# Kernel tuning notes

Hardware: AMD Instinct MI355X
Metric: run time of the kernel (lower is better)

Reference implementation:

```python
import jax, jax.numpy as jnp
import numpy as np

B, S, H, NH = 4, 1024, 1024, 16
DH = H // NH
EPS = 1e-12  # BERT layer_norm_eps


def layer_norm(x, scale, bias, eps=EPS):
    mu = jnp.mean(x, axis=-1, keepdims=True)
    var = jnp.var(x, axis=-1, keepdims=True)
    return (x - mu) / jnp.sqrt(var + eps) * scale + bias


def setup_inputs() -> dict:
    key = jax.random.key(0)
    ks = jax.random.split(key, 8)
    lin = lambda k: jax.random.normal(k, (H, H), jnp.float32) * 0.02
    zeros_h = jnp.zeros((H,), jnp.float32)
    return {
        "hidden_states": jax.random.normal(ks[0], (B, S, H), jnp.float32),
        "group_prob": jnp.zeros((B, S, S), jnp.float32),
        "attention_mask": jnp.ones((B, 1, S, S), jnp.int32),
        "Wq": lin(ks[1]), "bq": zeros_h,
        "Wk": lin(ks[2]), "bk": zeros_h,
        "Wv": lin(ks[3]), "bv": zeros_h,
        "gWq": lin(ks[4]), "gbq": zeros_h,
        "gWk": lin(ks[5]), "gbk": zeros_h,
        "g_ln_scale": jnp.ones((H,), jnp.float32), "g_ln_bias": zeros_h,
        "Wo": lin(ks[6]), "bo": zeros_h,
        "out_ln_scale": jnp.ones((H,), jnp.float32), "out_ln_bias": zeros_h,
    }


def _forward(hidden_states, group_prob, attention_mask, Wq, bq, Wk, bk, Wv, bv,
             gWq, gbq, gWk, gbk, g_ln_scale, g_ln_bias, Wo, bo,
             out_ln_scale, out_ln_bias):
    am = attention_mask.astype(jnp.int32)              # [B,1,S,S]
    a = jnp.eye(S, k=1, dtype=jnp.int32)               # superdiagonal
    b = jnp.eye(S, dtype=jnp.int32)                    # identity
    c = jnp.eye(S, k=-1, dtype=jnp.int32)              # subdiagonal
    tri = jnp.triu(jnp.ones((S, S), jnp.float32))      # upper tri incl diag

    # ---- GroupAttention (tree-transformer constituent priors) ----
    hs = layer_norm(hidden_states, g_ln_scale, g_ln_bias)
    gq = hs @ gWq.T + gbq
    gk = hs @ gWk.T + gbk
    g_scores = jnp.einsum('bqd,bkd->bqk', gq, gk) / jnp.float32(H)
    g_mask = (am & (a + c))[:, 0]                      # [B,S,S] tridiag band, no diag
    g_scores = jnp.where(g_mask == 0, -jnp.inf, g_scores)
    n_attn = jnp.nan_to_num(jax.nn.softmax(g_scores, axis=-1))
    n_attn = jnp.sqrt(n_attn * jnp.swapaxes(n_attn, -1, -2) + 1e-9)
    n_attn = group_prob + (1.0 - group_prob) * n_attn  # prior mixing
    t = jnp.where(a == 0, 0.0, jnp.log(n_attn + 1e-9)) @ tri
    g_attn = jnp.exp(tri @ t)
    strict_upper = tri.astype(jnp.int32) - b           # nonzero on strict upper tri
    g_attn = jnp.where(strict_upper == 0, 0.0, g_attn)
    g_attn = g_attn + jnp.swapaxes(g_attn, -1, -2) + jnp.where(b == 0, 1e-9, n_attn)
    break_prob = n_attn

    # ---- BertSelfAttention, mode 'L' ----
    def split_heads(x):
        return x.reshape(B, S, NH, DH).transpose(0, 2, 1, 3)  # [B,NH,S,DH]
    q = split_heads(hidden_states @ Wq.T + bq)
    k = split_heads(hidden_states @ Wk.T + bk)
    v = split_heads(hidden_states @ Wv.T + bv)
    scores = jnp.einsum('bhqd,bhkd->bhqk', q, k) / jnp.sqrt(jnp.float32(DH))
    keep = (am | b) != 0                               # diag always attended
    scores = jnp.where(keep, scores, -jnp.inf)
    probs = jax.nn.softmax(scores, axis=-1)
    probs = probs * g_attn[:, None]                    # group-prob reweighting
    ctx = jnp.einsum('bhqk,bhkd->bhqd', probs, v)
    ctx = ctx.transpose(0, 2, 1, 3).reshape(B, S, H)

    # ---- BertSelfOutput: dense + residual + LayerNorm ----
    out = layer_norm(ctx @ Wo.T + bo + hidden_states, out_ln_scale, out_ln_bias)
    return out, scores, g_attn, break_prob


def reference(hidden_states, group_prob, attention_mask, Wq, bq, Wk, bk, Wv, bv,
              gWq, gbq, gWk, gbk, g_ln_scale, g_ln_bias, Wo, bo,
              out_ln_scale, out_ln_bias):
    return _forward(hidden_states, group_prob, attention_mask, Wq, bq, Wk, bk,
                    Wv, bv, gWq, gbq, gWk, gbk, g_ln_scale, g_ln_bias, Wo, bo,
                    out_ln_scale, out_ln_bias)
```

## Files before the change

kernel.cpp:

```cpp
#include <hip/hip_runtime.h>
#include <math.h>

#define BB 4
#define S 1024
#define H 1024
#define NHD 16
#define DH 64
#define LN_EPS 1e-12f
#define SQ9 3.1622776601683795e-5f
#define NEG_INF (-__builtin_inff())

typedef unsigned short u16;
typedef unsigned int u32;
using bfrag = __attribute__((ext_vector_type(8))) short;
using f32x4 = __attribute__((ext_vector_type(4))) float;

typedef __attribute__((address_space(1))) void void_g;
typedef __attribute__((address_space(3))) void void_l;

__device__ __forceinline__ void gload16(const void* g, void* l) {
  __builtin_amdgcn_global_load_lds((void_g*)g, (void_l*)l, 16, 0, 0);
}

__device__ __forceinline__ u16 f2bf(float f) {
  u32 u = __builtin_bit_cast(u32, f);
  u32 r = (u + 0x7fffu + ((u >> 16) & 1u)) >> 16;
  return (u16)r;
}
__device__ __forceinline__ float bf2f(u32 b) {
  u32 u = b << 16;
  return __builtin_bit_cast(float, u);
}

__device__ __forceinline__ float block_sum256(float v, float* buf) {
#pragma unroll
  for (int o = 32; o > 0; o >>= 1) v += __shfl_down(v, o);
  if ((threadIdx.x & 63) == 0) buf[threadIdx.x >> 6] = v;
  __syncthreads();
  float r = buf[0] + buf[1] + buf[2] + buf[3];
  __syncthreads();
  return r;
}

__global__ __launch_bounds__(256) void cast_all_kernel(
    const float* __restrict__ Wq, const float* __restrict__ Wk, const float* __restrict__ Wv,
    const float* __restrict__ gWq, const float* __restrict__ gWk, const float* __restrict__ Wo,
    const float* __restrict__ hidden, u16* __restrict__ dst) {
  const int WQ = (H * H) / 4;
  int i = blockIdx.x * 256 + threadIdx.x;
  const float* src; int off;
  if      (i < 1 * WQ) { src = Wq;  off = 0; }
  else if (i < 2 * WQ) { src = Wk;  off = 1 * WQ; }
  else if (i < 3 * WQ) { src = Wv;  off = 2 * WQ; }
  else if (i < 4 * WQ) { src = gWq; off = 3 * WQ; }
  else if (i < 5 * WQ) { src = gWk; off = 4 * WQ; }
  else if (i < 6 * WQ) { src = Wo;  off = 5 * WQ; }
  else                 { src = hidden; off = 6 * WQ; }
  float4 v = reinterpret_cast<const float4*>(src)[i - off];
  u32 lo = (u32)f2bf(v.x) | ((u32)f2bf(v.y) << 16);
  u32 hi = (u32)f2bf(v.z) | ((u32)f2bf(v.w) << 16);
  reinterpret_cast<uint2*>(dst)[i] = make_uint2(lo, hi);
}

__global__ __launch_bounds__(256) void pack_mask_kernel(const int* __restrict__ am,
                                                        u32* __restrict__ amb) {
  size_t t = (size_t)blockIdx.x * 256 + threadIdx.x;
  int v = am[t] != 0;
  unsigned long long m = __ballot(v);
  int lane = threadIdx.x & 63;
  if (lane == 0)       amb[t >> 5] = (u32)m;
  else if (lane == 32) amb[t >> 5] = (u32)(m >> 32);
}

template <typename OutT>
__global__ __launch_bounds__(256) void ln_kernel(
    const float* __restrict__ x, const float* __restrict__ sc,
    const float* __restrict__ bi, OutT* __restrict__ y) {
  __shared__ float buf[4];
  size_t row = blockIdx.x;
  const float4 xv = reinterpret_cast<const float4*>(x + row * H)[threadIdx.x];
  float s  = xv.x + xv.y + xv.z + xv.w;
  float s2 = xv.x * xv.x + xv.y * xv.y + xv.z * xv.z + xv.w * xv.w;
  s  = block_sum256(s, buf);
  s2 = block_sum256(s2, buf);
  float mu  = s * (1.0f / H);
  float var = s2 * (1.0f / H) - mu * mu;
  float inv = rsqrtf(var + LN_EPS);
  const float4 sv = reinterpret_cast<const float4*>(sc)[threadIdx.x];
  const float4 bv = reinterpret_cast<const float4*>(bi)[threadIdx.x];
  float4 o;
  o.x = (xv.x - mu) * inv * sv.x + bv.x;
  o.y = (xv.y - mu) * inv * sv.y + bv.y;
  o.z = (xv.z - mu) * inv * sv.z + bv.z;
  o.w = (xv.w - mu) * inv * sv.w + bv.w;
  if constexpr (sizeof(OutT) == 2) {
    u32 lo = (u32)f2bf(o.x) | ((u32)f2bf(o.y) << 16);
    u32 hi = (u32)f2bf(o.z) | ((u32)f2bf(o.w) << 16);
    reinterpret_cast<uint2*>((u16*)y + row * H)[threadIdx.x] = make_uint2(lo, hi);
  } else {
    reinterpret_cast<float4*>((float*)y + row * H)[threadIdx.x] = o;
  }
}

__global__ __launch_bounds__(256) void gemm_bt3(
    const u16* __restrict__ A, const u16* __restrict__ Bcat,
    const float* __restrict__ b0, const float* __restrict__ b1, const float* __restrict__ b2,
    u16* __restrict__ o0, u16* __restrict__ o1, u16* __restrict__ o2) {
  __shared__ __align__(16) u16 Abuf[2][8192];
  __shared__ __align__(16) u16 Bbuf[2][8192];
  const int Kdim = H;
  int rowBlk = blockIdx.y * 128, colBlk = blockIdx.x * 128;
  int tid = threadIdx.x, wid = tid >> 6, l = tid & 63;
  int dr = l >> 3, sl = l & 7;
  int co = (sl ^ dr) << 3;
  const u16* Ag = A + (size_t)rowBlk * Kdim;
  const u16* Bg = Bcat + (size_t)colBlk * Kdim;
  f32x4 acc[4][4];
#pragma unroll
  for (int i = 0; i < 4; ++i)
#pragma unroll
    for (int j = 0; j < 4; ++j) acc[i][j] = (f32x4){0.f, 0.f, 0.f, 0.f};
#pragma unroll
  for (int i = 0; i < 4; ++i) {
    int L = wid * 4 + i;
    gload16(Ag + (size_t)(L * 8 + dr) * Kdim + co, &Abuf[0][L * 512]);
    gload16(Bg + (size_t)(L * 8 + dr) * Kdim + co, &Bbuf[0][L * 512]);
  }
  __syncthreads();
  int wm = wid >> 1, wn = wid & 1;
  const int nt = Kdim >> 6;
  int buf = 0;
  int sw = (l & 7) << 4;
  for (int t = 0; t < nt; ++t) {
    if (t + 1 < nt) {
      int k0 = (t + 1) << 6;
#pragma unroll
      for (int i = 0; i < 4; ++i) {
        int L = wid * 4 + i;
        gload16(Ag + (size_t)(L * 8 + dr) * Kdim + k0 + co, &Abuf[buf ^ 1][L * 512]);
        gload16(Bg + (size_t)(L * 8 + dr) * Kdim + k0 + co, &Bbuf[buf ^ 1][L * 512]);
      }
    }
    const char* Ab = (const char*)Abuf[buf];
    const char* Bb = (const char*)Bbuf[buf];
#pragma unroll
    for (int ks = 0; ks < 2; ++ks) {
      int kb = (ks * 64 + ((l >> 4) << 4)) ^ sw;
      bfrag af[4], bfv[4];
#pragma unroll
      for (int mi = 0; mi < 4; ++mi)
        af[mi] = *(const bfrag*)(Ab + (wm * 64 + mi * 16 + (l & 15)) * 128 + kb);
#pragma unroll
      for (int ni = 0; ni < 4; ++ni)
        bfv[ni] = *(const bfrag*)(Bb + (wn * 64 + ni * 16 + (l & 15)) * 128 + kb);
#pragma unroll
      for (int mi = 0; mi < 4; ++mi)
#pragma unroll
        for (int ni = 0; ni < 4; ++ni)
          acc[mi][ni] = __builtin_amdgcn_mfma_f32_16x16x32_bf16(af[mi], bfv[ni], acc[mi][ni], 0, 0, 0);
    }
    __syncthreads();
    buf ^= 1;
  }
  int which = colBlk >> 10;
  const float* bias = (which == 0) ? b0 : (which == 1) ? b1 : b2;
  u16* O = (which == 0) ? o0 : (which == 1) ? o1 : o2;
#pragma unroll
  for (int mi = 0; mi < 4; ++mi) {
#pragma unroll
    for (int ni = 0; ni < 4; ++ni) {
      int col = (colBlk + wn * 64 + ni * 16 + (l & 15)) & 1023;
      float bv = bias[col];
#pragma unroll
      for (int j = 0; j < 4; ++j) {
        int row = rowBlk + wm * 64 + mi * 16 + ((l >> 4) << 2) + j;
        O[(size_t)row * H + col] = f2bf(acc[mi][ni][j] + bv);
      }
    }
  }
}

__global__ __launch_bounds__(256) void gemm_dense(
    const u16* __restrict__ A, const u16* __restrict__ Bw,
    const float* __restrict__ bias, const float* __restrict__ resid,
    float* __restrict__ C) {
  __shared__ __align__(16) u16 Abuf[2][8192];
  __shared__ __align__(16) u16 Bbuf[2][8192];
  const int Kdim = H;
  int rowBlk = blockIdx.y * 128, colBlk = blockIdx.x * 128;
  int tid = threadIdx.x, wid = tid >> 6, l = tid & 63;
  int dr = l >> 3, sl = l & 7;
  int co = (sl ^ dr) << 3;
  const u16* Ag = A + (size_t)rowBlk * Kdim;
  const u16* Bg = Bw + (size_t)colBlk * Kdim;
  f32x4 acc[4][4];
#pragma unroll
  for (int i = 0; i < 4; ++i)
#pragma unroll
    for (int j = 0; j < 4; ++j) acc[i][j] = (f32x4){0.f, 0.f, 0.f, 0.f};
#pragma unroll
  for (int i = 0; i < 4; ++i) {
    int L = wid * 4 + i;
    gload16(Ag + (size_t)(L * 8 + dr) * Kdim + co, &Abuf[0][L * 512]);
    gload16(Bg + (size_t)(L * 8 + dr) * Kdim + co, &Bbuf[0][L * 512]);
  }
  __syncthreads();
  int wm = wid >> 1, wn = wid & 1;
  const int nt = Kdim >> 6;
  int buf = 0;
  int sw = (l & 7) << 4;
  for (int t = 0; t < nt; ++t) {
    if (t + 1 < nt) {
      int k0 = (t + 1) << 6;
#pragma unroll
      for (int i = 0; i < 4; ++i) {
        int L = wid * 4 + i;
        gload16(Ag + (size_t)(L * 8 + dr) * Kdim + k0 + co, &Abuf[buf ^ 1][L * 512]);
        gload16(Bg + (size_t)(L * 8 + dr) * Kdim + k0 + co, &Bbuf[buf ^ 1][L * 512]);
      }
    }
    const char* Ab = (const char*)Abuf[buf];
    const char* Bb = (const char*)Bbuf[buf];
#pragma unroll
    for (int ks = 0; ks < 2; ++ks) {
      int kb = (ks * 64 + ((l >> 4) << 4)) ^ sw;
      bfrag af[4], bfv[4];
#pragma unroll
      for (int mi = 0; mi < 4; ++mi)
        af[mi] = *(const bfrag*)(Ab + (wm * 64 + mi * 16 + (l & 15)) * 128 + kb);
#pragma unroll
      for (int ni = 0; ni < 4; ++ni)
        bfv[ni] = *(const bfrag*)(Bb + (wn * 64 + ni * 16 + (l & 15)) * 128 + kb);
#pragma unroll
      for (int mi = 0; mi < 4; ++mi)
#pragma unroll
        for (int ni = 0; ni < 4; ++ni)
          acc[mi][ni] = __builtin_amdgcn_mfma_f32_16x16x32_bf16(af[mi], bfv[ni], acc[mi][ni], 0, 0, 0);
    }
    __syncthreads();
    buf ^= 1;
  }
#pragma unroll
  for (int mi = 0; mi < 4; ++mi) {
#pragma unroll
    for (int ni = 0; ni < 4; ++ni) {
      int col = colBlk + wn * 64 + ni * 16 + (l & 15);
      float bv = bias[col];
#pragma unroll
      for (int j = 0; j < 4; ++j) {
        int row = rowBlk + wm * 64 + mi * 16 + ((l >> 4) << 2) + j;
        C[(size_t)row * H + col] = acc[mi][ni][j] + bv + resid[(size_t)row * H + col];
      }
    }
  }
}

__global__ __launch_bounds__(256) void band_dots_kernel(
    const u16* __restrict__ gq, const u16* __restrict__ gk,
    float* __restrict__ znext, float* __restrict__ zprev) {
  __shared__ float buf[4];
  size_t idx = blockIdx.x;
  int i = (int)(idx & (S - 1));
  uint2 q2 = reinterpret_cast<const uint2*>(gq + idx * H)[threadIdx.x];
  float q0 = bf2f(q2.x & 0xffff), q1 = bf2f(q2.x >> 16);
  float q2f = bf2f(q2.y & 0xffff), q3 = bf2f(q2.y >> 16);
  float dn = 0.f, dp = 0.f;
  if (i < S - 1) {
    uint2 k2 = reinterpret_cast<const uint2*>(gk + (idx + 1) * H)[threadIdx.x];
    dn = q0 * bf2f(k2.x & 0xffff) + q1 * bf2f(k2.x >> 16) +
         q2f * bf2f(k2.y & 0xffff) + q3 * bf2f(k2.y >> 16);
  }
  if (i > 0) {
    uint2 k2 = reinterpret_cast<const uint2*>(gk + (idx - 1) * H)[threadIdx.x];
    dp = q0 * bf2f(k2.x & 0xffff) + q1 * bf2f(k2.x >> 16) +
         q2f * bf2f(k2.y & 0xffff) + q3 * bf2f(k2.y >> 16);
  }
  dn = block_sum256(dn, buf);
  dp = block_sum256(dp, buf);
  if (threadIdx.x == 0) { znext[idx] = dn; zprev[idx] = dp; }
}

__global__ __launch_bounds__(1024) void band_prefix_kernel(
    const float* __restrict__ znext, const float* __restrict__ zprev,
    const int* __restrict__ am, const float* __restrict__ gp,
    float* __restrict__ sband, float* __restrict__ Cpre) {
  __shared__ float pd[S];
  __shared__ float scn[S];
  int b = blockIdx.x, i = threadIdx.x;
  size_t idx = (size_t)b * S + i;
  bool luv = (i < S - 1) && (am[((size_t)b * S + i) * S + i + 1] != 0);
  bool ldv = (i > 0) && (am[((size_t)b * S + i) * S + i - 1] != 0);
  float pf, pdn;
  if (!luv && !ldv) { pf = 0.f; pdn = 0.f; }
  else if (!ldv)    { pf = 1.f; pdn = 0.f; }
  else if (!luv)    { pf = 0.f; pdn = 1.f; }
  else {
    float lu = znext[idx] * (1.0f / (float)H);
    float ld = zprev[idx] * (1.0f / (float)H);
    float m = fmaxf(lu, ld);
    float eu = expf(lu - m), ed = expf(ld - m);
    float inv = 1.f / (eu + ed);
    pf = eu * inv; pdn = ed * inv;
  }
  pd[i] = pdn;
  __syncthreads();
  float sb = 0.f, L = 0.f;
  if (i < S - 1) {
    sb = sqrtf(pf * pd[i + 1] + 1e-9f);
    float gpv = gp[((size_t)b * S + i) * S + (i + 1)];
    float nm = gpv + (1.f - gpv) * sb;
    L = logf(nm + 1e-9f);
  }
  sband[idx] = sb;
  scn[i] = L;
  __syncthreads();
  for (int off = 1; off < S; off <<= 1) {
    float t = (i >= off) ? scn[i - off] : 0.f;
    __syncthreads();
    scn[i] += t;
    __syncthreads();
  }
  Cpre[idx] = (i > 0) ? scn[i - 1] : 0.f;
}

__global__ __launch_bounds__(256) void gattn_write_kernel(
    const float* __restrict__ gp, const float* __restrict__ sband,
    const float* __restrict__ Cpre, float* __restrict__ ga, float* __restrict__ brk) {
  __shared__ float Crow[S];
  __shared__ float Srow[S];
  size_t bi = blockIdx.x;
  int b = (int)(bi >> 10), i = (int)(bi & (S - 1));
  reinterpret_cast<float4*>(Crow)[threadIdx.x] =
      reinterpret_cast<const float4*>(Cpre + (size_t)b * S)[threadIdx.x];
  reinterpret_cast<float4*>(Srow)[threadIdx.x] =
      reinterpret_cast<const float4*>(sband + (size_t)b * S)[threadIdx.x];
  __syncthreads();
  float Ci = Crow[i];
  size_t rowoff = bi * S;
  const float4 g4 = reinterpret_cast<const float4*>(gp + rowoff)[threadIdx.x];
  const float gparr[4] = {g4.x, g4.y, g4.z, g4.w};
  float go[4], bo_[4];
#pragma unroll
  for (int j = 0; j < 4; ++j) {
    int k = threadIdx.x * 4 + j;
    float gpv = gparr[j];
    float gav;
    if (k == i) {
      gav = gpv + (1.f - gpv) * SQ9;
    } else {
      float d = (k > i) ? (Crow[k] - Ci) : (Ci - Crow[k]);
      gav = expf(d) + 1e-9f;
    }
    float sval = (k == i + 1) ? Srow[i] : ((k == i - 1) ? Srow[k] : SQ9);
    go[j]  = gav;
    bo_[j] = gpv + (1.f - gpv) * sval;
  }
  reinterpret_cast<float4*>(ga + rowoff)[threadIdx.x]  = make_float4(go[0], go[1], go[2], go[3]);
  f32x4 bo4 = (f32x4){bo_[0], bo_[1], bo_[2], bo_[3]};
  __builtin_nontemporal_store(bo4, reinterpret_cast<f32x4*>(brk + rowoff) + threadIdx.x);
}

__global__ __launch_bounds__(256) void transpose_v_kernel(
    const u16* __restrict__ v, u16* __restrict__ vt) {
  __shared__ __align__(16) u16 t[64][72];
  int sb = blockIdx.x, bh = blockIdx.y;
  int b = bh >> 4, h = bh & 15;
  int tid = threadIdx.x;
  int r = tid >> 3, c = (tid & 7) << 3;
#pragma unroll
  for (int p = 0; p < 2; ++p) {
    int row = p * 32 + r;
    uint4 d4 = *reinterpret_cast<const uint4*>(v + ((size_t)b * S + sb * 64 + row) * H + h * 64 + c);
    *reinterpret_cast<uint4*>(&t[row][c]) = d4;
  }
  __syncthreads();
  int d = tid >> 2, sq = (tid & 3) << 4;
  u32 w[8];
#pragma unroll
  for (int x = 0; x < 8; ++x)
    w[x] = (u32)t[sq + 2 * x][d] | ((u32)t[sq + 2 * x + 1][d] << 16);
  u16* dst = vt + ((size_t)bh * 64 + d) * S + sb * 64 + sq;
  reinterpret_cast<uint4*>(dst)[0] = make_uint4(w[0], w[1], w[2], w[3]);
  reinterpret_cast<uint4*>(dst)[1] = make_uint4(w[4], w[5], w[6], w[7]);
}

__global__ __launch_bounds__(256) void flash_kernel(
    const u16* __restrict__ q, const u16* __restrict__ k, const u16* __restrict__ vt,
    const u32* __restrict__ amb, const float* __restrict__ ga,
    float* __restrict__ scores, u16* __restrict__ ctx) {
  __shared__ __align__(16) u16 Qt[4096];
  __shared__ __align__(16) u16 Kt[2][4096];
  __shared__ __align__(16) u16 Vt[2][4096];
  __shared__ __align__(16) u16 Pt[4096];
  int qb = blockIdx.x, bh = blockIdx.y;
  int b = bh >> 4, h = bh & 15;
  int tid = threadIdx.x, wid = tid >> 6, l = tid & 63;
  int dr = l >> 3, sl = l & 7;
  int co = (sl ^ dr) << 3;
  const u16* qbase = q + ((size_t)b * S + qb * 64) * H + h * 64;
  const u16* kbase = k + (size_t)b * S * H + h * 64;
  const u16* vtb   = vt + (size_t)bh * 64 * S;
#pragma unroll
  for (int i = 0; i < 2; ++i) {
    int L = wid * 2 + i;
    gload16(qbase + (size_t)(L * 8 + dr) * H + co, &Qt[L * 512]);
    gload16(kbase + (size_t)(L * 8 + dr) * H + co, &Kt[0][L * 512]);
    gload16(vtb + (size_t)(L * 8 + dr) * S + co, &Vt[0][L * 512]);
  }
  __syncthreads();
  int sw = (l & 7) << 4;
  int qr = l & 15;
  bfrag qa[2];
#pragma unroll
  for (int ks = 0; ks < 2; ++ks) {
    int kb = (ks * 64 + ((l >> 4) << 4)) ^ sw;
    qa[ks] = *(const bfrag*)((const char*)Qt + (wid * 16 + qr) * 128 + kb);
  }
  float m_run[4], l_run[4];
  f32x4 oacc[4];
#pragma unroll
  for (int j = 0; j < 4; ++j) { m_run[j] = NEG_INF; l_run[j] = 0.f; }
#pragma unroll
  for (int nb = 0; nb < 4; ++nb) oacc[nb] = (f32x4){0.f, 0.f, 0.f, 0.f};
  int buf = 0;
  int rowg0 = qb * 64 + wid * 16 + ((l >> 4) << 2);
  for (int kt = 0; kt < 16; ++kt) {
    if (kt < 15) {
      const u16* kb2 = kbase + (size_t)((kt + 1) * 64) * H;
#pragma unroll
      for (int i = 0; i < 2; ++i) {
        int L = wid * 2 + i;
        gload16(kb2 + (size_t)(L * 8 + dr) * H + co, &Kt[buf ^ 1][L * 512]);
        gload16(vtb + (size_t)(L * 8 + dr) * S + (kt + 1) * 64 + co, &Vt[buf ^ 1][L * 512]);
      }
    }
    f32x4 acc[4];
#pragma unroll
    for (int nb = 0; nb < 4; ++nb) acc[nb] = (f32x4){0.f, 0.f, 0.f, 0.f};
#pragma unroll
    for (int ks = 0; ks < 2; ++ks) {
      int kb = (ks * 64 + ((l >> 4) << 4)) ^ sw;
#pragma unroll
      for (int nb = 0; nb < 4; ++nb) {
        bfrag bv = *(const bfrag*)((const char*)Kt[buf] + (nb * 16 + qr) * 128 + kb);
        acc[nb] = __builtin_amdgcn_mfma_f32_16x16x32_bf16(qa[ks], bv, acc[nb], 0, 0, 0);
      }
    }
    float vals[4][4];
    float tm[4] = {NEG_INF, NEG_INF, NEG_INF, NEG_INF};
#pragma unroll
    for (int j = 0; j < 4; ++j) {
      int row = rowg0 + j;
      const u32* amw = amb + ((size_t)b * S + row) * 32 + kt * 2;
      u32 w0 = amw[0], w1 = amw[1];
      float* srow = scores + ((size_t)bh * S + row) * S + kt * 64;
#pragma unroll
      for (int nb = 0; nb < 4; ++nb) {
        int col = nb * 16 + qr;
        int colg = kt * 64 + col;
        u32 word = (nb < 2) ? w0 : w1;
        int keep = (int)((word >> (col & 31)) & 1u) | (row == colg);
        float v = keep ? acc[nb][j] * 0.125f : NEG_INF;
        vals[nb][j] = v;
        __builtin_nontemporal_store(v, srow + col);
        tm[j] = fmaxf(tm[j], v);
      }
    }
#pragma unroll
    for (int j = 0; j < 4; ++j) {
#pragma unroll
      for (int o = 1; o < 16; o <<= 1) tm[j] = fmaxf(tm[j], __shfl_xor(tm[j], o));
    }
#pragma unroll
    for (int j = 0; j < 4; ++j) {
      int row = rowg0 + j;
      int prow = wid * 16 + ((l >> 4) << 2) + j;
      char* ptrow = (char*)Pt + prow * 128;
      int psw = (prow & 7) << 4;
      const float* garow = ga + ((size_t)b * S + row) * S + kt * 64;
      float mn = fmaxf(m_run[j], tm[j]);
      float p[4];
      float sc = 1.f, lsum = 0.f;
      if (mn > NEG_INF) {
        sc = expf(m_run[j] - mn);
#pragma unroll
        for (int nb = 0; nb < 4; ++nb) p[nb] = expf(vals[nb][j] - mn);
        lsum = p[0] + p[1] + p[2] + p[3];
      } else {
#pragma unroll
        for (int nb = 0; nb < 4; ++nb) p[nb] = 0.f;
      }
#pragma unroll
      for (int o = 1; o < 16; o <<= 1) lsum += __shfl_xor(lsum, o);
      m_run[j] = mn;
      l_run[j] = l_run[j] * sc + lsum;
#pragma unroll
      for (int nb = 0; nb < 4; ++nb) {
        float pg = p[nb] * garow[nb * 16 + qr];
        *(u16*)(ptrow + (((nb * 16 + qr) * 2) ^ psw)) = f2bf(pg);
        oacc[nb][j] *= sc;
      }
    }
#pragma unroll
    for (int ks = 0; ks < 2; ++ks) {
      int kb = (ks * 64 + ((l >> 4) << 4)) ^ sw;
      bfrag pa = *(const bfrag*)((const char*)Pt + (wid * 16 + qr) * 128 + kb);
#pragma unroll
      for (int nb = 0; nb < 4; ++nb) {
        bfrag vv = *(const bfrag*)((const char*)Vt[buf] + (nb * 16 + qr) * 128 + kb);
        oacc[nb] = __builtin_amdgcn_mfma_f32_16x16x32_bf16(pa, vv, oacc[nb], 0, 0, 0);
      }
    }
    __syncthreads();
    buf ^= 1;
  }
#pragma unroll
  for (int j = 0; j < 4; ++j) {
    int row = rowg0 + j;
    float ir = 1.f / l_run[j];
#pragma unroll
    for (int nb = 0; nb < 4; ++nb) {
      int d = nb * 16 + qr;
      ctx[((size_t)b * S + row) * H + h * 64 + d] = f2bf(oacc[nb][j] * ir);
    }
  }
}

extern "C" void kernel_launch(void* const* d_in, const int* in_sizes, int n_in,
                              void* d_out, int out_size, void* d_ws, size_t ws_size,
                              hipStream_t stream) {
  const float* hidden = (const float*)d_in[0];
  const float* gp     = (const float*)d_in[1];
  const int*   am     = (const int*)d_in[2];
  const float* Wq = (const float*)d_in[3];  const float* bq = (const float*)d_in[4];
  const float* Wk = (const float*)d_in[5];  const float* bk = (const float*)d_in[6];
  const float* Wv = (const float*)d_in[7];  const float* bv = (const float*)d_in[8];
  const float* gWq = (const float*)d_in[9]; const float* gbq = (const float*)d_in[10];
  const float* gWk = (const float*)d_in[11];const float* gbk = (const float*)d_in[12];
  const float* glns = (const float*)d_in[13]; const float* glnb = (const float*)d_in[14];
  const float* Wo = (const float*)d_in[15]; const float* bo = (const float*)d_in[16];
  const float* olns = (const float*)d_in[17]; const float* olnb = (const float*)d_in[18];

  float* out    = (float*)d_out;
  float* scores = out + (size_t)BB * S * H;
  float* gattn  = scores + (size_t)BB * NHD * S * S;
  float* brk    = gattn + (size_t)BB * S * S;

  const size_t MB = 1u << 20;
  char* w = (char*)d_ws;
  u16* Wqkvbf = (u16*)(w);
  u16* gWbf   = (u16*)(w + 6 * MB);
  u16* Wobf   = (u16*)(w + 10 * MB);
  u16* hbf    = (u16*)(w + 12 * MB);
  u16* ctxbf  = hbf;
  u16* hsbf   = (u16*)(w + 20 * MB);
  u16* vbf    = hsbf;
  u16* gqbf   = (u16*)(w + 28 * MB);
  u16* qbf    = gqbf;
  u16* gkbf   = (u16*)(w + 36 * MB);
  u16* kbf    = gkbf;
  u16* vtb    = (u16*)(w + 44 * MB);
  float* densef = (float*)(w + 20 * MB);
  u32* amb    = (u32*)(w + 52 * MB);
  float* znext  = (float*)(w + 53 * MB);
  float* zprev  = znext + BB * S;
  float* sbandA = zprev + BB * S;
  float* CpreA  = sbandA + BB * S;

  dim3 blk(256);
  dim3 agrid(S / 64, BB * NHD);

  cast_all_kernel<<<(6 * 262144 + 1048576) / 256, blk, 0, stream>>>(
      Wq, Wk, Wv, gWq, gWk, Wo, hidden, Wqkvbf);
  pack_mask_kernel<<<(BB * S * S) / 256, blk, 0, stream>>>(am, amb);

  ln_kernel<u16><<<BB * S, blk, 0, stream>>>(hidden, glns, glnb, hsbf);
  gemm_bt3<<<dim3(16, 32), blk, 0, stream>>>(hsbf, gWbf, gbq, gbk, nullptr,
                                             gqbf, gkbf, nullptr);
  band_dots_kernel<<<BB * S, blk, 0, stream>>>(gqbf, gkbf, znext, zprev);
  band_prefix_kernel<<<BB, 1024, 0, stream>>>(znext, zprev, am, gp, sbandA, CpreA);
  gattn_write_kernel<<<BB * S, blk, 0, stream>>>(gp, sbandA, CpreA, gattn, brk);

  gemm_bt3<<<dim3(24, 32), blk, 0, stream>>>(hbf, Wqkvbf, bq, bk, bv,
                                             qbf, kbf, vbf);
  transpose_v_kernel<<<agrid, blk, 0, stream>>>(vbf, vtb);
  flash_kernel<<<agrid, blk, 0, stream>>>(qbf, kbf, vtb, amb, gattn, scores, ctxbf);

  gemm_dense<<<dim3(8, 32), blk, 0, stream>>>(ctxbf, Wobf, bo, hidden, densef);
  ln_kernel<float><<<BB * S, blk, 0, stream>>>(densef, olns, olnb, out);
}
```

Before: 276.2 us.

## Fuse prep kernels, merge projection GEMMs with fused V transpose, add swizzles

Merges weight/hidden casting, mask packing and the group LayerNorm into one prep kernel, and runs the group and main QKV projections as a single GEMM launch whose V tiles are written already transposed through shared memory, removing the separate transpose kernel. Block-index swizzles are added to the GEMMs and the flash kernel to improve cache locality. The dense output is stored in bf16 before the final LayerNorm to cut traffic, at some precision cost in the pre-LN sum.

```diff
diff --git a/kernel.cpp b/kernel.cpp
--- a/kernel.cpp
+++ b/kernel.cpp
@@ -42,79 +42,86 @@
   return r;
 }
 
-__global__ __launch_bounds__(256) void cast_all_kernel(
+__global__ __launch_bounds__(256) void prep_kernel(
     const float* __restrict__ Wq, const float* __restrict__ Wk, const float* __restrict__ Wv,
-    const float* __restrict__ gWq, const float* __restrict__ gWk, const float* __restrict__ Wo,
-    const float* __restrict__ hidden, u16* __restrict__ dst) {
-  const int WQ = (H * H) / 4;
+    const float* __restrict__ gWq, const float* __restrict__ gWk,
+    const float* __restrict__ hidden, const int* __restrict__ am,
+    const float* __restrict__ glns, const float* __restrict__ glnb,
+    u16* __restrict__ dstW, u32* __restrict__ amb, u16* __restrict__ hsbf) {
+  __shared__ float buf[4];
+  int bid = blockIdx.x;
+  if (bid < 9216) {
+    const int WQ = 262144;
+    int i = bid * 256 + threadIdx.x;
+    const float* src; int off;
+    if      (i < 1 * WQ) { src = Wq;  off = 0; }
+    else if (i < 2 * WQ) { src = Wk;  off = 1 * WQ; }
+    else if (i < 3 * WQ) { src = Wv;  off = 2 * WQ; }
+    else if (i < 4 * WQ) { src = gWq; off = 3 * WQ; }
+    else if (i < 5 * WQ) { src = gWk; off = 4 * WQ; }
+    else                 { src = hidden; off = 5 * WQ; }
+    float4 v = reinterpret_cast<const float4*>(src)[i - off];
+    u32 lo = (u32)f2bf(v.x) | ((u32)f2bf(v.y) << 16);
+    u32 hi = (u32)f2bf(v.z) | ((u32)f2bf(v.w) << 16);
+    reinterpret_cast<uint2*>(dstW)[i] = make_uint2(lo, hi);
+  } else if (bid < 25600) {
+    size_t t = (size_t)(bid - 9216) * 256 + threadIdx.x;
+    int v = am[t] != 0;
+    unsigned long long m = __ballot(v);
+    int lane = threadIdx.x & 63;
+    if (lane == 0)       amb[t >> 5] = (u32)m;
+    else if (lane == 32) amb[t >> 5] = (u32)(m >> 32);
+  } else {
+    size_t row = bid - 25600;
+    const float4 xv = reinterpret_cast<const float4*>(hidden + row * H)[threadIdx.x];
+    float s  = xv.x + xv.y + xv.z + xv.w;
+    float s2 = xv.x * xv.x + xv.y * xv.y + xv.z * xv.z + xv.w * xv.w;
+    s  = block_sum256(s, buf);
+    s2 = block_sum256(s2, buf);
+    float mu  = s * (1.0f / H);
+    float var = s2 * (1.0f / H) - mu * mu;
+    float inv = rsqrtf(var + LN_EPS);
+    const float4 sv = reinterpret_cast<const float4*>(glns)[threadIdx.x];
+    const float4 bv = reinterpret_cast<const float4*>(glnb)[threadIdx.x];
+    float o0 = (xv.x - mu) * inv * sv.x + bv.x;
+    float o1 = (xv.y - mu) * inv * sv.y + bv.y;
+    float o2 = (xv.z - mu) * inv * sv.z + bv.z;
+    float o3 = (xv.w - mu) * inv * sv.w + bv.w;
+    u32 lo = (u32)f2bf(o0) | ((u32)f2bf(o1) << 16);
+    u32 hi = (u32)f2bf(o2) | ((u32)f2bf(o3) << 16);
+    reinterpret_cast<uint2*>(hsbf + row * H)[threadIdx.x] = make_uint2(lo, hi);
+  }
+}
+
+__global__ __launch_bounds__(256) void cast_wo_kernel(const float* __restrict__ Wo,
+                                                      u16* __restrict__ dst) {
   int i = blockIdx.x * 256 + threadIdx.x;
-  const float* src; int off;
-  if      (i < 1 * WQ) { src = Wq;  off = 0; }
-  else if (i < 2 * WQ) { src = Wk;  off = 1 * WQ; }
-  else if (i < 3 * WQ) { src = Wv;  off = 2 * WQ; }
-  else if (i < 4 * WQ) { src = gWq; off = 3 * WQ; }
-  else if (i < 5 * WQ) { src = gWk; off = 4 * WQ; }
-  else if (i < 6 * WQ) { src = Wo;  off = 5 * WQ; }
-  else                 { src = hidden; off = 6 * WQ; }
-  float4 v = reinterpret_cast<const float4*>(src)[i - off];
+  float4 v = reinterpret_cast<const float4*>(Wo)[i];
   u32 lo = (u32)f2bf(v.x) | ((u32)f2bf(v.y) << 16);
   u32 hi = (u32)f2bf(v.z) | ((u32)f2bf(v.w) << 16);
   reinterpret_cast<uint2*>(dst)[i] = make_uint2(lo, hi);
 }
 
-__global__ __launch_bounds__(256) void pack_mask_kernel(const int* __restrict__ am,
-                                                        u32* __restrict__ amb) {
-  size_t t = (size_t)blockIdx.x * 256 + threadIdx.x;
-  int v = am[t] != 0;
-  unsigned long long m = __ballot(v);
-  int lane = threadIdx.x & 63;
-  if (lane == 0)       amb[t >> 5] = (u32)m;
-  else if (lane == 32) amb[t >> 5] = (u32)(m >> 32);
-}
-
-template <typename OutT>
-__global__ __launch_bounds__(256) void ln_kernel(
-    const float* __restrict__ x, const float* __restrict__ sc,
-    const float* __restrict__ bi, OutT* __restrict__ y) {
-  __shared__ float buf[4];
-  size_t row = blockIdx.x;
-  const float4 xv = reinterpret_cast<const float4*>(x + row * H)[threadIdx.x];
-  float s  = xv.x + xv.y + xv.z + xv.w;
-  float s2 = xv.x * xv.x + xv.y * xv.y + xv.z * xv.z + xv.w * xv.w;
-  s  = block_sum256(s, buf);
-  s2 = block_sum256(s2, buf);
-  float mu  = s * (1.0f / H);
-  float var = s2 * (1.0f / H) - mu * mu;
-  float inv = rsqrtf(var + LN_EPS);
-  const float4 sv = reinterpret_cast<const float4*>(sc)[threadIdx.x];
-  const float4 bv = reinterpret_cast<const float4*>(bi)[threadIdx.x];
-  float4 o;
-  o.x = (xv.x - mu) * inv * sv.x + bv.x;
-  o.y = (xv.y - mu) * inv * sv.y + bv.y;
-  o.z = (xv.z - mu) * inv * sv.z + bv.z;
-  o.w = (xv.w - mu) * inv * sv.w + bv.w;
-  if constexpr (sizeof(OutT) == 2) {
-    u32 lo = (u32)f2bf(o.x) | ((u32)f2bf(o.y) << 16);
-    u32 hi = (u32)f2bf(o.z) | ((u32)f2bf(o.w) << 16);
-    reinterpret_cast<uint2*>((u16*)y + row * H)[threadIdx.x] = make_uint2(lo, hi);
-  } else {
-    reinterpret_cast<float4*>((float*)y + row * H)[threadIdx.x] = o;
-  }
-}
-
-__global__ __launch_bounds__(256) void gemm_bt3(
-    const u16* __restrict__ A, const u16* __restrict__ Bcat,
-    const float* __restrict__ b0, const float* __restrict__ b1, const float* __restrict__ b2,
-    u16* __restrict__ o0, u16* __restrict__ o1, u16* __restrict__ o2) {
-  __shared__ __align__(16) u16 Abuf[2][8192];
-  __shared__ __align__(16) u16 Bbuf[2][8192];
+__global__ __launch_bounds__(256) void mega_gemm(
+    const u16* __restrict__ hbf, const u16* __restrict__ hsbf,
+    const u16* __restrict__ Wcat,
+    const float* __restrict__ bq, const float* __restrict__ bk, const float* __restrict__ bv,
+    const float* __restrict__ gbq, const float* __restrict__ gbk,
+    u16* __restrict__ q, u16* __restrict__ k, u16* __restrict__ vt,
+    u16* __restrict__ gq, u16* __restrict__ gk) {
+  __shared__ __align__(16) u16 SM[32768];
   const int Kdim = H;
-  int rowBlk = blockIdx.y * 128, colBlk = blockIdx.x * 128;
+  int fid = blockIdx.x + blockIdx.y * 40;
+  int swz = (fid & 7) * 160 + (fid >> 3);
+  int lx = swz % 40, ly = swz / 40;
+  int which = lx >> 3;
+  const u16* A = (which < 3) ? hbf : hsbf;
+  int rowBlk = ly * 128, colBlk = lx * 128;
   int tid = threadIdx.x, wid = tid >> 6, l = tid & 63;
   int dr = l >> 3, sl = l & 7;
   int co = (sl ^ dr) << 3;
   const u16* Ag = A + (size_t)rowBlk * Kdim;
-  const u16* Bg = Bcat + (size_t)colBlk * Kdim;
+  const u16* Bg = Wcat + (size_t)colBlk * Kdim;
   f32x4 acc[4][4];
 #pragma unroll
   for (int i = 0; i < 4; ++i)
@@ -123,8 +130,8 @@
 #pragma unroll
   for (int i = 0; i < 4; ++i) {
     int L = wid * 4 + i;
-    gload16(Ag + (size_t)(L * 8 + dr) * Kdim + co, &Abuf[0][L * 512]);
-    gload16(Bg + (size_t)(L * 8 + dr) * Kdim + co, &Bbuf[0][L * 512]);
+    gload16(Ag + (size_t)(L * 8 + dr) * Kdim + co, &SM[L * 512]);
+    gload16(Bg + (size_t)(L * 8 + dr) * Kdim + co, &SM[16384 + L * 512]);
   }
   __syncthreads();
   int wm = wid >> 1, wn = wid & 1;
@@ -134,15 +141,16 @@
   for (int t = 0; t < nt; ++t) {
     if (t + 1 < nt) {
       int k0 = (t + 1) << 6;
+      int dstoff = (buf ^ 1) * 8192;
 #pragma unroll
       for (int i = 0; i < 4; ++i) {
         int L = wid * 4 + i;
-        gload16(Ag + (size_t)(L * 8 + dr) * Kdim + k0 + co, &Abuf[buf ^ 1][L * 512]);
-        gload16(Bg + (size_t)(L * 8 + dr) * Kdim + k0 + co, &Bbuf[buf ^ 1][L * 512]);
-      }
-    }
-    const char* Ab = (const char*)Abuf[buf];
-    const char* Bb = (const char*)Bbuf[buf];
+        gload16(Ag + (size_t)(L * 8 + dr) * Kdim + k0 + co, &SM[dstoff + L * 512]);
+        gload16(Bg + (size_t)(L * 8 + dr) * Kdim + k0 + co, &SM[16384 + dstoff + L * 512]);
+      }
+    }
+    const char* Ab = (const char*)&SM[buf * 8192];
+    const char* Bb = (const char*)&SM[16384 + buf * 8192];
 #pragma unroll
     for (int ks = 0; ks < 2; ++ks) {
       int kb = (ks * 64 + ((l >> 4) << 4)) ^ sw;
@@ -162,19 +170,45 @@
     __syncthreads();
     buf ^= 1;
   }
-  int which = colBlk >> 10;
-  const float* bias = (which == 0) ? b0 : (which == 1) ? b1 : b2;
-  u16* O = (which == 0) ? o0 : (which == 1) ? o1 : o2;
-#pragma unroll
-  for (int mi = 0; mi < 4; ++mi) {
-#pragma unroll
-    for (int ni = 0; ni < 4; ++ni) {
-      int col = (colBlk + wn * 64 + ni * 16 + (l & 15)) & 1023;
-      float bv = bias[col];
-#pragma unroll
-      for (int j = 0; j < 4; ++j) {
-        int row = rowBlk + wm * 64 + mi * 16 + ((l >> 4) << 2) + j;
-        O[(size_t)row * H + col] = f2bf(acc[mi][ni][j] + bv);
+  const float* bias = (which == 0) ? bq : (which == 1) ? bk : (which == 2) ? bv
+                      : (which == 3) ? gbq : gbk;
+  if (which == 2) {
+    u16* T = SM;
+#pragma unroll
+    for (int mi = 0; mi < 4; ++mi) {
+#pragma unroll
+      for (int ni = 0; ni < 4; ++ni) {
+        int c = wn * 64 + ni * 16 + (l & 15);
+        float bvv = bias[(colBlk & 1023) + c];
+        int tokb = wm * 64 + mi * 16 + ((l >> 4) << 2);
+        u32 w0 = (u32)f2bf(acc[mi][ni][0] + bvv) | ((u32)f2bf(acc[mi][ni][1] + bvv) << 16);
+        u32 w1 = (u32)f2bf(acc[mi][ni][2] + bvv) | ((u32)f2bf(acc[mi][ni][3] + bvv) << 16);
+        *(u32*)&T[c * 144 + tokb]     = w0;
+        *(u32*)&T[c * 144 + tokb + 2] = w1;
+      }
+    }
+    __syncthreads();
+    int col = tid >> 1, th = tid & 1;
+    int g = (colBlk & 1023) + col;
+    int bb = rowBlk >> 10;
+    int s0 = (rowBlk & 1023) + th * 64;
+    const uint4* src = (const uint4*)&T[col * 144 + th * 64];
+    u16* dst = vt + ((size_t)(bb * 1024 + g)) * S + s0;
+#pragma unroll
+    for (int i = 0; i < 8; ++i) reinterpret_cast<uint4*>(dst)[i] = src[i];
+  } else {
+    u16* O = (which == 0) ? q : (which == 1) ? k : (which == 3) ? gq : gk;
+#pragma unroll
+    for (int mi = 0; mi < 4; ++mi) {
+#pragma unroll
+      for (int ni = 0; ni < 4; ++ni) {
+        int col = (colBlk + wn * 64 + ni * 16 + (l & 15)) & 1023;
+        float bvv = bias[col];
+#pragma unroll
+        for (int j = 0; j < 4; ++j) {
+          int row = rowBlk + wm * 64 + mi * 16 + ((l >> 4) << 2) + j;
+          O[(size_t)row * H + col] = f2bf(acc[mi][ni][j] + bvv);
+        }
       }
     }
   }
@@ -183,11 +217,13 @@
 __global__ __launch_bounds__(256) void gemm_dense(
     const u16* __restrict__ A, const u16* __restrict__ Bw,
     const float* __restrict__ bias, const float* __restrict__ resid,
-    float* __restrict__ C) {
-  __shared__ __align__(16) u16 Abuf[2][8192];
-  __shared__ __align__(16) u16 Bbuf[2][8192];
+    u16* __restrict__ C) {
+  __shared__ __align__(16) u16 SM[32768];
   const int Kdim = H;
-  int rowBlk = blockIdx.y * 128, colBlk = blockIdx.x * 128;
+  int fid = blockIdx.x + blockIdx.y * 8;
+  int swz = (fid & 7) * 32 + (fid >> 3);
+  int lx = swz & 7, ly = swz >> 3;
+  int rowBlk = ly * 128, colBlk = lx * 128;
   int tid = threadIdx.x, wid = tid >> 6, l = tid & 63;
   int dr = l >> 3, sl = l & 7;
   int co = (sl ^ dr) << 3;
@@ -201,8 +237,8 @@
 #pragma unroll
   for (int i = 0; i < 4; ++i) {
     int L = wid * 4 + i;
-    gload16(Ag + (size_t)(L * 8 + dr) * Kdim + co, &Abuf[0][L * 512]);
-    gload16(Bg + (size_t)(L * 8 + dr) * Kdim + co, &Bbuf[0][L * 512]);
+    gload16(Ag + (size_t)(L * 8 + dr) * Kdim + co, &SM[L * 512]);
+    gload16(Bg + (size_t)(L * 8 + dr) * Kdim + co, &SM[16384 + L * 512]);
   }
   __syncthreads();
   int wm = wid >> 1, wn = wid & 1;
@@ -212,15 +248,16 @@
   for (int t = 0; t < nt; ++t) {
     if (t + 1 < nt) {
       int k0 = (t + 1) << 6;
+      int dstoff = (buf ^ 1) * 8192;
 #pragma unroll
       for (int i = 0; i < 4; ++i) {
         int L = wid * 4 + i;
-        gload16(Ag + (size_t)(L * 8 + dr) * Kdim + k0 + co, &Abuf[buf ^ 1][L * 512]);
-        gload16(Bg + (size_t)(L * 8 + dr) * Kdim + k0 + co, &Bbuf[buf ^ 1][L * 512]);
-      }
-    }
-    const char* Ab = (const char*)Abuf[buf];
-    const char* Bb = (const char*)Bbuf[buf];
+        gload16(Ag + (size_t)(L * 8 + dr) * Kdim + k0 + co, &SM[dstoff + L * 512]);
+        gload16(Bg + (size_t)(L * 8 + dr) * Kdim + k0 + co, &SM[16384 + dstoff + L * 512]);
+      }
+    }
+    const char* Ab = (const char*)&SM[buf * 8192];
+    const char* Bb = (const char*)&SM[16384 + buf * 8192];
 #pragma unroll
     for (int ks = 0; ks < 2; ++ks) {
       int kb = (ks * 64 + ((l >> 4) << 4)) ^ sw;
@@ -245,11 +282,11 @@
 #pragma unroll
     for (int ni = 0; ni < 4; ++ni) {
       int col = colBlk + wn * 64 + ni * 16 + (l & 15);
-      float bv = bias[col];
+      float bvv = bias[col];
 #pragma unroll
       for (int j = 0; j < 4; ++j) {
         int row = rowBlk + wm * 64 + mi * 16 + ((l >> 4) << 2) + j;
-        C[(size_t)row * H + col] = acc[mi][ni][j] + bv + resid[(size_t)row * H + col];
+        C[(size_t)row * H + col] = f2bf(acc[mi][ni][j] + bvv + resid[(size_t)row * H + col]);
       }
     }
   }
@@ -360,30 +397,6 @@
   __builtin_nontemporal_store(bo4, reinterpret_cast<f32x4*>(brk + rowoff) + threadIdx.x);
 }
 
-__global__ __launch_bounds__(256) void transpose_v_kernel(
-    const u16* __restrict__ v, u16* __restrict__ vt) {
-  __shared__ __align__(16) u16 t[64][72];
-  int sb = blockIdx.x, bh = blockIdx.y;
-  int b = bh >> 4, h = bh & 15;
-  int tid = threadIdx.x;
-  int r = tid >> 3, c = (tid & 7) << 3;
-#pragma unroll
-  for (int p = 0; p < 2; ++p) {
-    int row = p * 32 + r;
-    uint4 d4 = *reinterpret_cast<const uint4*>(v + ((size_t)b * S + sb * 64 + row) * H + h * 64 + c);
-    *reinterpret_cast<uint4*>(&t[row][c]) = d4;
-  }
-  __syncthreads();
-  int d = tid >> 2, sq = (tid & 3) << 4;
-  u32 w[8];
-#pragma unroll
-  for (int x = 0; x < 8; ++x)
-    w[x] = (u32)t[sq + 2 * x][d] | ((u32)t[sq + 2 * x + 1][d] << 16);
-  u16* dst = vt + ((size_t)bh * 64 + d) * S + sb * 64 + sq;
-  reinterpret_cast<uint4*>(dst)[0] = make_uint4(w[0], w[1], w[2], w[3]);
-  reinterpret_cast<uint4*>(dst)[1] = make_uint4(w[4], w[5], w[6], w[7]);
-}
-
 __global__ __launch_bounds__(256) void flash_kernel(
     const u16* __restrict__ q, const u16* __restrict__ k, const u16* __restrict__ vt,
     const u32* __restrict__ amb, const float* __restrict__ ga,
@@ -392,7 +405,9 @@
   __shared__ __align__(16) u16 Kt[2][4096];
   __shared__ __align__(16) u16 Vt[2][4096];
   __shared__ __align__(16) u16 Pt[4096];
-  int qb = blockIdx.x, bh = blockIdx.y;
+  int fid = blockIdx.x + blockIdx.y * 16;
+  int swz = (fid & 7) * 128 + (fid >> 3);
+  int qb = swz & 15, bh = swz >> 4;
   int b = bh >> 4, h = bh & 15;
   int tid = threadIdx.x, wid = tid >> 6, l = tid & 63;
   int dr = l >> 3, sl = l & 7;
@@ -524,6 +539,31 @@
       ctx[((size_t)b * S + row) * H + h * 64 + d] = f2bf(oacc[nb][j] * ir);
     }
   }
+}
+
+__global__ __launch_bounds__(256) void ln_bf_kernel(
+    const u16* __restrict__ x, const float* __restrict__ sc,
+    const float* __restrict__ bi, float* __restrict__ y) {
+  __shared__ float buf[4];
+  size_t row = blockIdx.x;
+  uint2 xv = reinterpret_cast<const uint2*>(x + row * H)[threadIdx.x];
+  float x0 = bf2f(xv.x & 0xffff), x1 = bf2f(xv.x >> 16);
+  float x2 = bf2f(xv.y & 0xffff), x3 = bf2f(xv.y >> 16);
+  float s  = x0 + x1 + x2 + x3;
+  float s2 = x0 * x0 + x1 * x1 + x2 * x2 + x3 * x3;
+  s  = block_sum256(s, buf);
+  s2 = block_sum256(s2, buf);
+  float mu  = s * (1.0f / H);
+  float var = s2 * (1.0f / H) - mu * mu;
+  float inv = rsqrtf(var + LN_EPS);
+  const float4 sv = reinterpret_cast<const float4*>(sc)[threadIdx.x];
+  const float4 bv = reinterpret_cast<const float4*>(bi)[threadIdx.x];
+  float4 o;
+  o.x = (x0 - mu) * inv * sv.x + bv.x;
+  o.y = (x1 - mu) * inv * sv.y + bv.y;
+  o.z = (x2 - mu) * inv * sv.z + bv.z;
+  o.w = (x3 - mu) * inv * sv.w + bv.w;
+  reinterpret_cast<float4*>(y + row * H)[threadIdx.x] = o;
 }
 
 extern "C" void kernel_launch(void* const* d_in, const int* in_sizes, int n_in,
@@ -548,44 +588,39 @@
 
   const size_t MB = 1u << 20;
   char* w = (char*)d_ws;
-  u16* Wqkvbf = (u16*)(w);
-  u16* gWbf   = (u16*)(w + 6 * MB);
-  u16* Wobf   = (u16*)(w + 10 * MB);
-  u16* hbf    = (u16*)(w + 12 * MB);
-  u16* ctxbf  = hbf;
-  u16* hsbf   = (u16*)(w + 20 * MB);
-  u16* vbf    = hsbf;
-  u16* gqbf   = (u16*)(w + 28 * MB);
-  u16* qbf    = gqbf;
-  u16* gkbf   = (u16*)(w + 36 * MB);
-  u16* kbf    = gkbf;
-  u16* vtb    = (u16*)(w + 44 * MB);
-  float* densef = (float*)(w + 20 * MB);
-  u32* amb    = (u32*)(w + 52 * MB);
-  float* znext  = (float*)(w + 53 * MB);
+  u16* Wcat  = (u16*)(w);
+  u16* hbf   = (u16*)(w + 10 * MB);
+  u16* ctxbf = hbf;
+  u16* hsbf  = (u16*)(w + 18 * MB);
+  u16* Wobf  = hsbf;
+  u16* qbf   = (u16*)(w + 26 * MB);
+  u16* kbf   = (u16*)(w + 34 * MB);
+  u16* vtb   = (u16*)(w + 42 * MB);
+  u16* gqbf  = (u16*)(w + 50 * MB);
+  u16* densebf = gqbf;
+  u16* gkbf  = (u16*)(w + 58 * MB);
+  u32* amb   = (u32*)(w + 66 * MB);
+  float* znext  = (float*)(w + 66 * MB + 512 * 1024);
   float* zprev  = znext + BB * S;
   float* sbandA = zprev + BB * S;
   float* CpreA  = sbandA + BB * S;
 
   dim3 blk(256);
-  dim3 agrid(S / 64, BB * NHD);
-
-  cast_all_kernel<<<(6 * 262144 + 1048576) / 256, blk, 0, stream>>>(
-      Wq, Wk, Wv, gWq, gWk, Wo, hidden, Wqkvbf);
-  pack_mask_kernel<<<(BB * S * S) / 256, blk, 0, stream>>>(am, amb);
-
-  ln_kernel<u16><<<BB * S, blk, 0, stream>>>(hidden, glns, glnb, hsbf);
-  gemm_bt3<<<dim3(16, 32), blk, 0, stream>>>(hsbf, gWbf, gbq, gbk, nullptr,
-                                             gqbf, gkbf, nullptr);
+
+  prep_kernel<<<29696, blk, 0, stream>>>(Wq, Wk, Wv, gWq, gWk, hidden, am,
+                                         glns, glnb, Wcat, amb, hsbf);
+
+  mega_gemm<<<dim3(40, 32), blk, 0, stream>>>(hbf, hsbf, Wcat,
+                                              bq, bk, bv, gbq, gbk,
+                                              qbf, kbf, vtb, gqbf, gkbf);
+  cast_wo_kernel<<<1024, blk, 0, stream>>>(Wo, Wobf);
+
   band_dots_kernel<<<BB * S, blk, 0, stream>>>(gqbf, gkbf, znext, zprev);
   band_prefix_kernel<<<BB, 1024, 0, stream>>>(znext, zprev, am, gp, sbandA, CpreA);
   gattn_write_kernel<<<BB * S, blk, 0, stream>>>(gp, sbandA, CpreA, gattn, brk);
 
-  gemm_bt3<<<dim3(24, 32), blk, 0, stream>>>(hbf, Wqkvbf, bq, bk, bv,
-                                             qbf, kbf, vbf);
-  transpose_v_kernel<<<agrid, blk, 0, stream>>>(vbf, vtb);
-  flash_kernel<<<agrid, blk, 0, stream>>>(qbf, kbf, vtb, amb, gattn, scores, ctxbf);
-
-  gemm_dense<<<dim3(8, 32), blk, 0, stream>>>(ctxbf, Wobf, bo, hidden, densef);
-  ln_kernel<float><<<BB * S, blk, 0, stream>>>(densef, olns, olnb, out);
-}
+  flash_kernel<<<dim3(16, 64), blk, 0, stream>>>(qbf, kbf, vtb, amb, gattn, scores, ctxbf);
+
+  gemm_dense<<<dim3(8, 32), blk, 0, stream>>>(ctxbf, Wobf, bo, hidden, densebf);
+  ln_bf_kernel<<<BB * S, blk, 0, stream>>>(densebf, olns, olnb, out);
+}
```

New measurement: 269.6 us. 1.02x faster.
